# Kernel tuning notes

Hardware: AMD Instinct MI355X
Metric: run time of the kernel (lower is better)

The kernel has to match this reference:

```python
import jax, jax.numpy as jnp
import numpy as np

PI_2 = 3.14159 / 2  # matches torch module constant (not exact pi/2, keeps tan finite)
EPS_SUM = 1e-07
EPS_COS = 1e-08  # torch F.cosine_similarity default eps


def setup_inputs() -> dict:
    key = jax.random.key(0)
    k1, k2 = jax.random.split(key)
    B, N, C, H, W = 16, 2000, 512, 7, 7
    # memory is uniform-initialized then sum-normalized per cube, as in __init__
    memory = jax.random.uniform(k1, (N, C, H, W), dtype=jnp.float32)
    memory = memory / (jnp.sum(memory, axis=(1, 2, 3), keepdims=True) + EPS_SUM)
    key_t = jax.random.uniform(k2, (B, C, H, W), dtype=jnp.float32)
    return {"key": key_t, "memory": memory}


def reference(key, memory):
    # _normalize: divide key by its per-sample sum
    k = key / (jnp.sum(key, axis=(1, 2, 3), keepdims=True) + EPS_SUM)
    B = k.shape[0]
    N = memory.shape[0]
    kf = k.reshape(B, -1)            # [B, D], D = C*H*W
    mf = memory.reshape(N, -1)       # [N, D]
    # cosine similarity (torch clamps each norm to eps)
    dots = jnp.einsum('bd,nd->bn', kf, mf)                       # [B, N]
    kn = jnp.maximum(jnp.linalg.norm(kf, axis=-1), EPS_COS)      # [B]
    mn = jnp.maximum(jnp.linalg.norm(mf, axis=-1), EPS_COS)      # [N]
    cos = dots / (kn[:, None] * mn[None, :])
    w = jax.nn.softmax(jnp.tan(cos * PI_2), axis=1)              # [B, N]
    # read: sum over memory cubes weighted by address w
    return jnp.einsum('bn,nchw->bchw', w, memory)                # [B, C, H, W]
```

## Files before the change

### kernel.cpp

```cpp
#include <hip/hip_runtime.h>
#include <math.h>

#define B 16
#define N 2000
#define D 25088
#define D4 6272
#define PI2 1.570795f
#define KC 16
#define KSPAN (D / KC)
#define KTILES (KSPAN / 32)
#define NT (D / 32)
#define NCHUNK 10
#define NPER (N / NCHUNK)

typedef __attribute__((ext_vector_type(8))) short short8;
typedef __attribute__((ext_vector_type(4))) float f32x4;

__device__ __forceinline__ float wave_sum(float v) {
#pragma unroll
    for (int off = 32; off > 0; off >>= 1) v += __shfl_xor(v, off, 64);
    return v;
}
__device__ __forceinline__ float wave_max(float v) {
#pragma unroll
    for (int off = 32; off > 0; off >>= 1) v = fmaxf(v, __shfl_xor(v, off, 64));
    return v;
}

__global__ void k_split(const float* __restrict__ key, unsigned short* __restrict__ ksw) {
    const int g    = blockIdx.x * 256 + threadIdx.x;
    const int tile = g >> 6, lane = g & 63;
    const int m = lane & 15, quad = lane >> 4;
    const float* src = key + (size_t)m * D + tile * 32 + quad * 8;
    float4 x0 = *(const float4*)src;
    float4 x1 = *(const float4*)(src + 4);
    float xs[8] = {x0.x, x0.y, x0.z, x0.w, x1.x, x1.y, x1.z, x1.w};
    unsigned short h[8], l[8];
#pragma unroll
    for (int j = 0; j < 8; ++j) {
        unsigned int u = __float_as_uint(xs[j]);
        h[j] = (unsigned short)(u >> 16);
        float lo = xs[j] - __uint_as_float(u & 0xFFFF0000u);
        l[j] = (unsigned short)(__float_as_uint(lo) >> 16);
    }
    unsigned short* dh = ksw + ((size_t)tile * 64 + lane) * 8;
    unsigned short* dl = ksw + ((size_t)(NT + tile) * 64 + lane) * 8;
#pragma unroll
    for (int j = 0; j < 8; ++j) { dh[j] = h[j]; dl[j] = l[j]; }
}

__global__ __launch_bounds__(256) void k_dots(const float* __restrict__ mem,
                                              const unsigned short* __restrict__ ksw,
                                              float* __restrict__ dpart,
                                              float* __restrict__ mpart) {
    const int tid  = threadIdx.x;
    const int lane = tid & 63;
    const int wave = tid >> 6;
    const int n0   = blockIdx.x * 16;
    const int kc   = blockIdx.y * 4 + wave;
    const int nrow = lane & 15, quad = lane >> 4;

    const float* mrow = mem + (size_t)(n0 + nrow) * D + kc * KSPAN + quad * 8;
    const short8* kh = (const short8*)(ksw + ((size_t)(kc * KTILES) * 64 + lane) * 8);
    const short8* kl = (const short8*)(ksw + ((size_t)(NT + kc * KTILES) * 64 + lane) * 8);

    f32x4 ahh = {0.f, 0.f, 0.f, 0.f};
    f32x4 ahl = ahh, alh = ahh;
    float msq = 0.f;

    for (int t = 0; t < KTILES; ++t) {
        float4 x0 = *(const float4*)(mrow + t * 32);
        float4 x1 = *(const float4*)(mrow + t * 32 + 4);
        short8 ah = kh[(size_t)t * 64];
        short8 al = kl[(size_t)t * 64];
        float xs[8] = {x0.x, x0.y, x0.z, x0.w, x1.x, x1.y, x1.z, x1.w};
        short8 bh, bl;
#pragma unroll
        for (int j = 0; j < 8; ++j) {
            unsigned int u = __float_as_uint(xs[j]);
            bh[j] = (short)(u >> 16);
            float lo = xs[j] - __uint_as_float(u & 0xFFFF0000u);
            bl[j] = (short)(__float_as_uint(lo) >> 16);
            msq = fmaf(xs[j], xs[j], msq);
        }
        ahh = __builtin_amdgcn_mfma_f32_16x16x32_bf16(ah, bh, ahh, 0, 0, 0);
        ahl = __builtin_amdgcn_mfma_f32_16x16x32_bf16(ah, bl, ahl, 0, 0, 0);
        alh = __builtin_amdgcn_mfma_f32_16x16x32_bf16(al, bh, alh, 0, 0, 0);
    }

    f32x4 dt;
#pragma unroll
    for (int r = 0; r < 4; ++r) dt[r] = ahh[r] + ahl[r] + alh[r];
#pragma unroll
    for (int r = 0; r < 4; ++r)
        dpart[((size_t)kc * B + quad * 4 + r) * N + n0 + nrow] = dt[r];

    msq += __shfl_xor(msq, 16, 64);
    msq += __shfl_xor(msq, 32, 64);
    if (quad == 0) mpart[(size_t)kc * N + n0 + nrow] = msq;
}

__global__ __launch_bounds__(256, 2) void k_softmax(const float4* __restrict__ key,
                                                    const float* __restrict__ dpart,
                                                    const float* __restrict__ mpart,
                                                    float* __restrict__ w) {
    const int b = blockIdx.x, tid = threadIdx.x;
    const int wv = tid >> 6, ln = tid & 63;
    __shared__ float t[N];
    __shared__ float redA[4], redB[4], redC[4];

    float s = 0.f;
    for (int i = tid; i < D4; i += 256) {
        float4 v = key[(size_t)b * D4 + i];
        s = fmaf(v.x, v.x, s); s = fmaf(v.y, v.y, s);
        s = fmaf(v.z, v.z, s); s = fmaf(v.w, v.w, s);
    }
    s = wave_sum(s);
    if (ln == 0) redA[wv] = s;
    __syncthreads();
    const float kn = fmaxf(sqrtf(redA[0] + redA[1] + redA[2] + redA[3]), 1e-8f);

    float mx = -1e30f;
    for (int n = tid; n < N; n += 256) {
        float ds = 0.f, ms = 0.f;
#pragma unroll
        for (int kc = 0; kc < KC; ++kc) {
            ds += dpart[((size_t)kc * B + b) * N + n];
            ms += mpart[(size_t)kc * N + n];
        }
        float mn = fmaxf(sqrtf(ms), 1e-8f);
        float tv = tanf(ds / (kn * mn) * PI2);
        t[n] = tv;
        mx = fmaxf(mx, tv);
    }
    mx = wave_max(mx);
    if (ln == 0) redB[wv] = mx;
    __syncthreads();
    mx = fmaxf(fmaxf(redB[0], redB[1]), fmaxf(redB[2], redB[3]));

    float sum = 0.f;
    for (int n = tid; n < N; n += 256) {
        float e = expf(t[n] - mx);
        t[n] = e;
        sum += e;
    }
    sum = wave_sum(sum);
    if (ln == 0) redC[wv] = sum;
    __syncthreads();
    sum = redC[0] + redC[1] + redC[2] + redC[3];
    const float inv = 1.f / sum;
    for (int n = tid; n < N; n += 256) w[(size_t)b * N + n] = t[n] * inv;
}

__global__ __launch_bounds__(128) void k_out_p(const float4* __restrict__ mem,
                                               const float* __restrict__ w,
                                               float4* __restrict__ part) {
    const int tid = threadIdx.x;
    const int d4  = blockIdx.x * 128 + tid;
    const int n0  = blockIdx.y * NPER;

    __shared__ float wt[B * NPER];
    for (int i = tid; i < B * NPER; i += 128)
        wt[i] = w[(size_t)(i / NPER) * N + n0 + (i % NPER)];
    __syncthreads();

    const float4* mp = mem + (size_t)n0 * D4 + d4;
    float4 acc[B];
#pragma unroll
    for (int b = 0; b < B; ++b) acc[b] = make_float4(0.f, 0.f, 0.f, 0.f);

    for (int n = 0; n < NPER; n += 8) {
        float4 mv[8];
#pragma unroll
        for (int u = 0; u < 8; ++u) mv[u] = mp[(size_t)(n + u) * D4];
#pragma unroll
        for (int b = 0; b < B; ++b) {
            float4 a = acc[b];
#pragma unroll
            for (int u = 0; u < 8; ++u) {
                const float wv = wt[b * NPER + n + u];
                a.x = fmaf(wv, mv[u].x, a.x); a.y = fmaf(wv, mv[u].y, a.y);
                a.z = fmaf(wv, mv[u].z, a.z); a.w = fmaf(wv, mv[u].w, a.w);
            }
            acc[b] = a;
        }
    }
#pragma unroll
    for (int b = 0; b < B; ++b)
        part[((size_t)blockIdx.y * B + b) * D4 + d4] = acc[b];
}

__global__ void k_reduce(const float4* __restrict__ part, float4* __restrict__ out) {
    const int i = blockIdx.x * 256 + threadIdx.x;
    float4 s = part[i];
#pragma unroll
    for (int c = 1; c < NCHUNK; ++c) {
        float4 p = part[(size_t)c * B * D4 + i];
        s.x += p.x; s.y += p.y; s.z += p.z; s.w += p.w;
    }
    out[i] = s;
}

__global__ __launch_bounds__(128) void k_out_atomic(const float4* __restrict__ mem,
                                                    const float* __restrict__ w,
                                                    float* __restrict__ out) {
    const int tid = threadIdx.x;
    const int d4  = blockIdx.x * 128 + tid;
    const int n0  = blockIdx.y * NPER;
    __shared__ float wt[B * NPER];
    for (int i = tid; i < B * NPER; i += 128)
        wt[i] = w[(size_t)(i / NPER) * N + n0 + (i % NPER)];
    __syncthreads();
    const float4* mp = mem + (size_t)n0 * D4 + d4;
    float4 acc[B];
#pragma unroll
    for (int b = 0; b < B; ++b) acc[b] = make_float4(0.f, 0.f, 0.f, 0.f);
    for (int n = 0; n < NPER; n += 8) {
        float4 mv[8];
#pragma unroll
        for (int u = 0; u < 8; ++u) mv[u] = mp[(size_t)(n + u) * D4];
#pragma unroll
        for (int b = 0; b < B; ++b) {
            float4 a = acc[b];
#pragma unroll
            for (int u = 0; u < 8; ++u) {
                const float wv = wt[b * NPER + n + u];
                a.x = fmaf(wv, mv[u].x, a.x); a.y = fmaf(wv, mv[u].y, a.y);
                a.z = fmaf(wv, mv[u].z, a.z); a.w = fmaf(wv, mv[u].w, a.w);
            }
            acc[b] = a;
        }
    }
#pragma unroll
    for (int b = 0; b < B; ++b) {
        float* op = out + (size_t)b * D + (size_t)d4 * 4;
        unsafeAtomicAdd(op + 0, acc[b].x);
        unsafeAtomicAdd(op + 1, acc[b].y);
        unsafeAtomicAdd(op + 2, acc[b].z);
        unsafeAtomicAdd(op + 3, acc[b].w);
    }
}

extern "C" void kernel_launch(void* const* d_in, const int* in_sizes, int n_in,
                              void* d_out, int out_size, void* d_ws, size_t ws_size,
                              hipStream_t stream) {
    const float* key = (const float*)d_in[0];
    const float* mem = (const float*)d_in[1];
    float* out = (float*)d_out;

    float* ws = (float*)d_ws;
    unsigned short* ksw = (unsigned short*)ws;
    float* dpart = ws + 401408;
    float* mpart = dpart + (size_t)KC * B * N;
    float* w     = mpart + (size_t)KC * N;
    float* part  = w + (size_t)B * N;
    const size_t need_full = (size_t)(401408 + KC * B * N + KC * N + B * N + NCHUNK * B * D) * 4;

    k_split<<<dim3(NT * 64 / 256), 256, 0, stream>>>(key, ksw);
    k_dots<<<dim3(N / 16, 4), 256, 0, stream>>>(mem, ksw, dpart, mpart);
    k_softmax<<<dim3(B), 256, 0, stream>>>((const float4*)key, dpart, mpart, w);
    if (ws_size >= need_full) {
        k_out_p<<<dim3(D4 / 128, NCHUNK), 128, 0, stream>>>((const float4*)mem, w, (float4*)part);
        k_reduce<<<dim3(B * D4 / 256), 256, 0, stream>>>((const float4*)part, (float4*)out);
    } else {
        hipMemsetAsync(d_out, 0, (size_t)B * D * sizeof(float), stream);
        k_out_atomic<<<dim3(D4 / 128, NCHUNK), 128, 0, stream>>>((const float4*)mem, w, out);
    }
}
```

Measured before the change: 383.0 us.

## Prefetch loads in dots and output kernels, fuse key norm, retune chunking

The dots kernel and the output-accumulation kernel now software-prefetch the next tile's memory and key fragments into registers, so loads overlap with the MFMA and FMA work. The fp32-to-bf16 hi/lo split uses byte-permute instructions instead of per-element shifts. The key's squared norm is computed in the split kernel with atomics, which removes a full re-read of the key in the softmax kernel. The output stage uses 25 N-chunks and 256-thread blocks instead of 10 chunks and 128 threads. That raises parallelism but makes the partial buffer and the reduction pass larger, and it needs a larger workspace or the atomic fallback is taken.

```diff
diff --git a/kernel.cpp b/kernel.cpp
--- a/kernel.cpp
+++ b/kernel.cpp
@@ -10,11 +10,16 @@
 #define KSPAN (D / KC)
 #define KTILES (KSPAN / 32)
 #define NT (D / 32)
-#define NCHUNK 10
+#define NCHUNK 25
 #define NPER (N / NCHUNK)
+#define SELHI 0x07060302u
 
 typedef __attribute__((ext_vector_type(8))) short short8;
 typedef __attribute__((ext_vector_type(4))) float f32x4;
+typedef unsigned int uint;
+
+union pk { uint4 u; short8 s; };
+__device__ __forceinline__ short8 as_s8(uint4 u) { pk p; p.u = u; return p.s; }
 
 __device__ __forceinline__ float wave_sum(float v) {
 #pragma unroll
@@ -27,32 +32,59 @@
     return v;
 }
 
-__global__ void k_split(const float* __restrict__ key, unsigned short* __restrict__ ksw) {
-    const int g    = blockIdx.x * 256 + threadIdx.x;
+__device__ __forceinline__ void cvt_hilo(const float4& a, const float4& b,
+                                         short8& hi, short8& lo, float& msq) {
+    float xs[8] = {a.x, a.y, a.z, a.w, b.x, b.y, b.z, b.w};
+    uint lu[8];
+#pragma unroll
+    for (int j = 0; j < 8; ++j) {
+        uint u = __float_as_uint(xs[j]);
+        float lof = xs[j] - __uint_as_float(u & 0xffff0000u);
+        lu[j] = __float_as_uint(lof);
+        msq = fmaf(xs[j], xs[j], msq);
+    }
+    uint4 h, l;
+    h.x = __builtin_amdgcn_perm(__float_as_uint(xs[1]), __float_as_uint(xs[0]), SELHI);
+    h.y = __builtin_amdgcn_perm(__float_as_uint(xs[3]), __float_as_uint(xs[2]), SELHI);
+    h.z = __builtin_amdgcn_perm(__float_as_uint(xs[5]), __float_as_uint(xs[4]), SELHI);
+    h.w = __builtin_amdgcn_perm(__float_as_uint(xs[7]), __float_as_uint(xs[6]), SELHI);
+    l.x = __builtin_amdgcn_perm(lu[1], lu[0], SELHI);
+    l.y = __builtin_amdgcn_perm(lu[3], lu[2], SELHI);
+    l.z = __builtin_amdgcn_perm(lu[5], lu[4], SELHI);
+    l.w = __builtin_amdgcn_perm(lu[7], lu[6], SELHI);
+    hi = as_s8(h); lo = as_s8(l);
+}
+
+__global__ void k_split(const float* __restrict__ key, unsigned short* __restrict__ ksw,
+                        float* __restrict__ kn2) {
+    const int tid  = threadIdx.x;
+    const int g    = blockIdx.x * 256 + tid;
     const int tile = g >> 6, lane = g & 63;
     const int m = lane & 15, quad = lane >> 4;
     const float* src = key + (size_t)m * D + tile * 32 + quad * 8;
     float4 x0 = *(const float4*)src;
     float4 x1 = *(const float4*)(src + 4);
-    float xs[8] = {x0.x, x0.y, x0.z, x0.w, x1.x, x1.y, x1.z, x1.w};
-    unsigned short h[8], l[8];
-#pragma unroll
-    for (int j = 0; j < 8; ++j) {
-        unsigned int u = __float_as_uint(xs[j]);
-        h[j] = (unsigned short)(u >> 16);
-        float lo = xs[j] - __uint_as_float(u & 0xFFFF0000u);
-        l[j] = (unsigned short)(__float_as_uint(lo) >> 16);
-    }
-    unsigned short* dh = ksw + ((size_t)tile * 64 + lane) * 8;
-    unsigned short* dl = ksw + ((size_t)(NT + tile) * 64 + lane) * 8;
-#pragma unroll
-    for (int j = 0; j < 8; ++j) { dh[j] = h[j]; dl[j] = l[j]; }
-}
-
-__global__ __launch_bounds__(256) void k_dots(const float* __restrict__ mem,
-                                              const unsigned short* __restrict__ ksw,
-                                              float* __restrict__ dpart,
-                                              float* __restrict__ mpart) {
+    short8 hi, lo;
+    float ssq = 0.f;
+    cvt_hilo(x0, x1, hi, lo, ssq);
+    pk ph; ph.s = hi;
+    pk pl; pl.s = lo;
+    *(uint4*)(ksw + ((size_t)tile * 64 + lane) * 8)        = ph.u;
+    *(uint4*)(ksw + ((size_t)(NT + tile) * 64 + lane) * 8) = pl.u;
+
+    ssq += __shfl_xor(ssq, 16, 64);
+    ssq += __shfl_xor(ssq, 32, 64);
+    __shared__ float lds[4][16];
+    if (quad == 0) lds[tid >> 6][m] = ssq;
+    __syncthreads();
+    if (tid < 16)
+        atomicAdd(&kn2[tid], lds[0][tid] + lds[1][tid] + lds[2][tid] + lds[3][tid]);
+}
+
+__global__ __launch_bounds__(256, 2) void k_dots(const float* __restrict__ mem,
+                                                 const unsigned short* __restrict__ ksw,
+                                                 float* __restrict__ dpart,
+                                                 float* __restrict__ mpart) {
     const int tid  = threadIdx.x;
     const int lane = tid & 63;
     const int wave = tid >> 6;
@@ -60,32 +92,32 @@
     const int kc   = blockIdx.y * 4 + wave;
     const int nrow = lane & 15, quad = lane >> 4;
 
-    const float* mrow = mem + (size_t)(n0 + nrow) * D + kc * KSPAN + quad * 8;
-    const short8* kh = (const short8*)(ksw + ((size_t)(kc * KTILES) * 64 + lane) * 8);
-    const short8* kl = (const short8*)(ksw + ((size_t)(NT + kc * KTILES) * 64 + lane) * 8);
+    const float4* mrow4 = (const float4*)(mem + (size_t)(n0 + nrow) * D + kc * KSPAN) + quad * 2;
+    const uint4* khp = (const uint4*)(ksw + ((size_t)(kc * KTILES) * 64 + lane) * 8);
+    const uint4* klp = (const uint4*)(ksw + ((size_t)(NT + kc * KTILES) * 64 + lane) * 8);
 
     f32x4 ahh = {0.f, 0.f, 0.f, 0.f};
     f32x4 ahl = ahh, alh = ahh;
     float msq = 0.f;
 
+    float4 c0 = mrow4[0], c1 = mrow4[1];
+    uint4 kah = khp[0],  kal = klp[0];
+
     for (int t = 0; t < KTILES; ++t) {
-        float4 x0 = *(const float4*)(mrow + t * 32);
-        float4 x1 = *(const float4*)(mrow + t * 32 + 4);
-        short8 ah = kh[(size_t)t * 64];
-        short8 al = kl[(size_t)t * 64];
-        float xs[8] = {x0.x, x0.y, x0.z, x0.w, x1.x, x1.y, x1.z, x1.w};
+        const int tn = (t + 1 < KTILES) ? t + 1 : t;
+        float4 p0 = mrow4[(size_t)tn * 8];
+        float4 p1 = mrow4[(size_t)tn * 8 + 1];
+        uint4 pah = khp[(size_t)tn * 64];
+        uint4 pal = klp[(size_t)tn * 64];
+
         short8 bh, bl;
-#pragma unroll
-        for (int j = 0; j < 8; ++j) {
-            unsigned int u = __float_as_uint(xs[j]);
-            bh[j] = (short)(u >> 16);
-            float lo = xs[j] - __uint_as_float(u & 0xFFFF0000u);
-            bl[j] = (short)(__float_as_uint(lo) >> 16);
-            msq = fmaf(xs[j], xs[j], msq);
-        }
+        cvt_hilo(c0, c1, bh, bl, msq);
+        short8 ah = as_s8(kah), al = as_s8(kal);
         ahh = __builtin_amdgcn_mfma_f32_16x16x32_bf16(ah, bh, ahh, 0, 0, 0);
         ahl = __builtin_amdgcn_mfma_f32_16x16x32_bf16(ah, bl, ahl, 0, 0, 0);
         alh = __builtin_amdgcn_mfma_f32_16x16x32_bf16(al, bh, alh, 0, 0, 0);
+
+        c0 = p0; c1 = p1; kah = pah; kal = pal;
     }
 
     f32x4 dt;
@@ -100,25 +132,16 @@
     if (quad == 0) mpart[(size_t)kc * N + n0 + nrow] = msq;
 }
 
-__global__ __launch_bounds__(256, 2) void k_softmax(const float4* __restrict__ key,
+__global__ __launch_bounds__(256, 2) void k_softmax(const float* __restrict__ kn2,
                                                     const float* __restrict__ dpart,
                                                     const float* __restrict__ mpart,
                                                     float* __restrict__ w) {
     const int b = blockIdx.x, tid = threadIdx.x;
     const int wv = tid >> 6, ln = tid & 63;
     __shared__ float t[N];
-    __shared__ float redA[4], redB[4], redC[4];
-
-    float s = 0.f;
-    for (int i = tid; i < D4; i += 256) {
-        float4 v = key[(size_t)b * D4 + i];
-        s = fmaf(v.x, v.x, s); s = fmaf(v.y, v.y, s);
-        s = fmaf(v.z, v.z, s); s = fmaf(v.w, v.w, s);
-    }
-    s = wave_sum(s);
-    if (ln == 0) redA[wv] = s;
-    __syncthreads();
-    const float kn = fmaxf(sqrtf(redA[0] + redA[1] + redA[2] + redA[3]), 1e-8f);
+    __shared__ float redB[4], redC[4];
+
+    const float kn = fmaxf(sqrtf(kn2[b]), 1e-8f);
 
     float mx = -1e30f;
     for (int n = tid; n < N; n += 256) {
@@ -152,23 +175,79 @@
     for (int n = tid; n < N; n += 256) w[(size_t)b * N + n] = t[n] * inv;
 }
 
-__global__ __launch_bounds__(128) void k_out_p(const float4* __restrict__ mem,
-                                               const float* __restrict__ w,
-                                               float4* __restrict__ part) {
+__global__ __launch_bounds__(256, 2) void k_out_p(const float4* __restrict__ mem,
+                                                  const float* __restrict__ w,
+                                                  float4* __restrict__ part) {
     const int tid = threadIdx.x;
-    const int d4  = blockIdx.x * 128 + tid;
+    const int d4  = blockIdx.x * 256 + tid;
     const int n0  = blockIdx.y * NPER;
 
     __shared__ float wt[B * NPER];
-    for (int i = tid; i < B * NPER; i += 128)
+    for (int i = tid; i < B * NPER; i += 256)
         wt[i] = w[(size_t)(i / NPER) * N + n0 + (i % NPER)];
     __syncthreads();
+    if (d4 >= D4) return;
 
     const float4* mp = mem + (size_t)n0 * D4 + d4;
     float4 acc[B];
 #pragma unroll
     for (int b = 0; b < B; ++b) acc[b] = make_float4(0.f, 0.f, 0.f, 0.f);
 
+    float4 cur[8];
+#pragma unroll
+    for (int u = 0; u < 8; ++u) cur[u] = mp[(size_t)u * D4];
+
+#pragma unroll
+    for (int g = 0; g < NPER / 8; ++g) {
+        const int gn = (g + 1 < NPER / 8) ? g + 1 : g;
+        float4 nxt[8];
+#pragma unroll
+        for (int u = 0; u < 8; ++u) nxt[u] = mp[(size_t)(gn * 8 + u) * D4];
+#pragma unroll
+        for (int b = 0; b < B; ++b) {
+            float4 a = acc[b];
+#pragma unroll
+            for (int u = 0; u < 8; ++u) {
+                const float wv = wt[b * NPER + g * 8 + u];
+                a.x = fmaf(wv, cur[u].x, a.x); a.y = fmaf(wv, cur[u].y, a.y);
+                a.z = fmaf(wv, cur[u].z, a.z); a.w = fmaf(wv, cur[u].w, a.w);
+            }
+            acc[b] = a;
+        }
+#pragma unroll
+        for (int u = 0; u < 8; ++u) cur[u] = nxt[u];
+    }
+#pragma unroll
+    for (int b = 0; b < B; ++b)
+        part[((size_t)blockIdx.y * B + b) * D4 + d4] = acc[b];
+}
+
+__global__ void k_reduce(const float4* __restrict__ part, float4* __restrict__ out) {
+    const int i = blockIdx.x * 256 + threadIdx.x;
+    float4 s = part[i];
+#pragma unroll
+    for (int c = 1; c < NCHUNK; ++c) {
+        float4 p = part[(size_t)c * B * D4 + i];
+        s.x += p.x; s.y += p.y; s.z += p.z; s.w += p.w;
+    }
+    out[i] = s;
+}
+
+__global__ __launch_bounds__(256, 2) void k_out_atomic(const float4* __restrict__ mem,
+                                                       const float* __restrict__ w,
+                                                       float* __restrict__ out) {
+    const int tid = threadIdx.x;
+    const int d4  = blockIdx.x * 256 + tid;
+    const int n0  = blockIdx.y * NPER;
+    __shared__ float wt[B * NPER];
+    for (int i = tid; i < B * NPER; i += 256)
+        wt[i] = w[(size_t)(i / NPER) * N + n0 + (i % NPER)];
+    __syncthreads();
+    if (d4 >= D4) return;
+    const float4* mp = mem + (size_t)n0 * D4 + d4;
+    float4 acc[B];
+#pragma unroll
+    for (int b = 0; b < B; ++b) acc[b] = make_float4(0.f, 0.f, 0.f, 0.f);
     for (int n = 0; n < NPER; n += 8) {
         float4 mv[8];
 #pragma unroll
@@ -186,52 +265,6 @@
         }
     }
 #pragma unroll
-    for (int b = 0; b < B; ++b)
-        part[((size_t)blockIdx.y * B + b) * D4 + d4] = acc[b];
-}
-
-__global__ void k_reduce(const float4* __restrict__ part, float4* __restrict__ out) {
-    const int i = blockIdx.x * 256 + threadIdx.x;
-    float4 s = part[i];
-#pragma unroll
-    for (int c = 1; c < NCHUNK; ++c) {
-        float4 p = part[(size_t)c * B * D4 + i];
-        s.x += p.x; s.y += p.y; s.z += p.z; s.w += p.w;
-    }
-    out[i] = s;
-}
-
-__global__ __launch_bounds__(128) void k_out_atomic(const float4* __restrict__ mem,
-                                                    const float* __restrict__ w,
-                                                    float* __restrict__ out) {
-    const int tid = threadIdx.x;
-    const int d4  = blockIdx.x * 128 + tid;
-    const int n0  = blockIdx.y * NPER;
-    __shared__ float wt[B * NPER];
-    for (int i = tid; i < B * NPER; i += 128)
-        wt[i] = w[(size_t)(i / NPER) * N + n0 + (i % NPER)];
-    __syncthreads();
-    const float4* mp = mem + (size_t)n0 * D4 + d4;
-    float4 acc[B];
-#pragma unroll
-    for (int b = 0; b < B; ++b) acc[b] = make_float4(0.f, 0.f, 0.f, 0.f);
-    for (int n = 0; n < NPER; n += 8) {
-        float4 mv[8];
-#pragma unroll
-        for (int u = 0; u < 8; ++u) mv[u] = mp[(size_t)(n + u) * D4];
-#pragma unroll
-        for (int b = 0; b < B; ++b) {
-            float4 a = acc[b];
-#pragma unroll
-            for (int u = 0; u < 8; ++u) {
-                const float wv = wt[b * NPER + n + u];
-                a.x = fmaf(wv, mv[u].x, a.x); a.y = fmaf(wv, mv[u].y, a.y);
-                a.z = fmaf(wv, mv[u].z, a.z); a.w = fmaf(wv, mv[u].w, a.w);
-            }
-            acc[b] = a;
-        }
-    }
-#pragma unroll
     for (int b = 0; b < B; ++b) {
         float* op = out + (size_t)b * D + (size_t)d4 * 4;
         unsafeAtomicAdd(op + 0, acc[b].x);
@@ -252,18 +285,21 @@
     unsigned short* ksw = (unsigned short*)ws;
     float* dpart = ws + 401408;
     float* mpart = dpart + (size_t)KC * B * N;
-    float* w     = mpart + (size_t)KC * N;
+    float* kn2   = mpart + (size_t)KC * N;
+    float* w     = kn2 + 16;
     float* part  = w + (size_t)B * N;
-    const size_t need_full = (size_t)(401408 + KC * B * N + KC * N + B * N + NCHUNK * B * D) * 4;
-
-    k_split<<<dim3(NT * 64 / 256), 256, 0, stream>>>(key, ksw);
+    const size_t need_full =
+        (size_t)(401408 + (size_t)KC * B * N + KC * N + 16 + B * N + (size_t)NCHUNK * B * D) * 4;
+
+    hipMemsetAsync(kn2, 0, 16 * sizeof(float), stream);
+    k_split<<<dim3(NT * 64 / 256), 256, 0, stream>>>(key, ksw, kn2);
     k_dots<<<dim3(N / 16, 4), 256, 0, stream>>>(mem, ksw, dpart, mpart);
-    k_softmax<<<dim3(B), 256, 0, stream>>>((const float4*)key, dpart, mpart, w);
+    k_softmax<<<dim3(B), 256, 0, stream>>>(kn2, dpart, mpart, w);
     if (ws_size >= need_full) {
-        k_out_p<<<dim3(D4 / 128, NCHUNK), 128, 0, stream>>>((const float4*)mem, w, (float4*)part);
+        k_out_p<<<dim3((D4 + 255) / 256, NCHUNK), 256, 0, stream>>>((const float4*)mem, w, (float4*)part);
         k_reduce<<<dim3(B * D4 / 256), 256, 0, stream>>>((const float4*)part, (float4*)out);
     } else {
         hipMemsetAsync(d_out, 0, (size_t)B * D * sizeof(float), stream);
-        k_out_atomic<<<dim3(D4 / 128, NCHUNK), 128, 0, stream>>>((const float4*)mem, w, out);
-    }
-}
+        k_out_atomic<<<dim3((D4 + 255) / 256, NCHUNK), 256, 0, stream>>>((const float4*)mem, w, out);
+    }
+}
```

Measured after the change: 359.3 us. 1.07x faster.
